# Optimization experiments

Measured on AMD Instinct MI355X. Metric: run time of the kernel, lower is better.

The kernel has to match this reference:

```python
import jax, jax.numpy as jnp
import numpy as np

D, H, L, FF, IN, OUT, S, B = 512, 8, 6, 2048, 32, 3, 512, 32


def setup_inputs() -> dict:
    key = jax.random.key(0)
    ks = iter(jax.random.split(key, 32))
    w = lambda shape: jax.random.normal(next(ks), shape, jnp.float32) * 0.02
    z = lambda shape: jnp.zeros(shape, jnp.float32)
    o = lambda shape: jnp.ones(shape, jnp.float32)
    return {
        'x': jax.random.normal(next(ks), (B, S, IN), jnp.float32),
        'w_in': w((IN, D)), 'b_in': z((D,)), 'g_in': o((D,)), 'be_in': z((D,)),
        'w_qkv': w((L, D, 3 * D)), 'b_qkv': z((L, 3 * D)),
        'w_out': w((L, D, D)), 'b_out': z((L, D)),
        'g1': o((L, D)), 'be1': z((L, D)),
        'w_ff1': w((L, D, FF)), 'b_ff1': z((L, FF)),
        'w_ff2': w((L, FF, D)), 'b_ff2': z((L, D)),
        'g2': o((L, D)), 'be2': z((L, D)),
        'w_h1': w((D, D // 2)), 'b_h1': z((D // 2,)),
        'w_h2': w((D // 2, OUT)), 'b_h2': z((OUT,)),
    }


def _layer_norm(x, g, b, eps=1e-5):
    mu = jnp.mean(x, axis=-1, keepdims=True)
    var = jnp.mean(jnp.square(x - mu), axis=-1, keepdims=True)
    return (x - mu) / jnp.sqrt(var + eps) * g + b


def _gelu(x):
    return jax.nn.gelu(x, approximate=False)  # torch nn.GELU default (erf)


def _pos_encoding(seq_len, d_model):
    pos = jnp.arange(seq_len, dtype=jnp.float32)[:, None]
    div = jnp.exp(jnp.arange(0, d_model, 2, dtype=jnp.float32) * (-np.log(10000.0) / d_model))
    pe = jnp.zeros((seq_len, d_model), jnp.float32)
    pe = pe.at[:, 0::2].set(jnp.sin(pos * div))
    pe = pe.at[:, 1::2].set(jnp.cos(pos * div))
    return pe


def reference(x, w_in, b_in, g_in, be_in, w_qkv, b_qkv, w_out, b_out,
              g1, be1, w_ff1, b_ff1, w_ff2, b_ff2, g2, be2,
              w_h1, b_h1, w_h2, b_h2):
    b, s, _ = x.shape
    d = w_in.shape[1]
    hd = d // H
    scale = hd ** -0.5

    # input projection: Linear -> LayerNorm -> GELU (dropout = identity at eval)
    h = _gelu(_layer_norm(x @ w_in + b_in, g_in, be_in))
    h = h + _pos_encoding(s, d)

    causal_mask = jnp.triu(jnp.ones((s, s), bool), 1)  # True above diagonal = future

    for l in range(w_qkv.shape[0]):
        qkv = (h @ w_qkv[l] + b_qkv[l]).reshape(b, s, 3, H, hd)
        q, k, v = qkv[:, :, 0], qkv[:, :, 1], qkv[:, :, 2]  # [b, s, H, hd]
        scores = jnp.einsum('bihd,bjhd->bhij', q, k) * scale
        scores = jnp.where(causal_mask, -jnp.inf, scores)
        attn = jax.nn.softmax(scores, axis=-1)
        o = jnp.einsum('bhij,bjhd->bihd', attn, v).reshape(b, s, d)
        o = o @ w_out[l] + b_out[l]
        h = _layer_norm(h + o, g1[l], be1[l])
        f = _gelu(h @ w_ff1[l] + b_ff1[l]) @ w_ff2[l] + b_ff2[l]
        h = _layer_norm(h + f, g2[l], be2[l])

    logits = _gelu(h @ w_h1 + b_h1) @ w_h2 + b_h2  # [b, s, OUT]
    return logits[:, -1, :]  # last position only
```

## Files before the change

kernel.cpp:

```cpp
#include <hip/hip_runtime.h>
#include <hip/hip_bf16.h>
#include <math.h>

#define D_   512
#define H_   8
#define HD_  64
#define L_   6
#define FF_  2048
#define IN_  32
#define OUT_ 3
#define S_   512
#define B_   32
#define M_   (B_ * S_)

typedef __attribute__((ext_vector_type(8))) short short8;
typedef __attribute__((ext_vector_type(4))) float floatx4;

__device__ __forceinline__ float gelu_f(float x) {
    const float ax = fabsf(x) * 0.70710678118654752f;
    const float t = __builtin_amdgcn_rcpf(fmaf(0.3275911f, ax, 1.0f));
    float p = fmaf(1.061405429f, t, -1.453152027f);
    p = fmaf(p, t, 1.421413741f);
    p = fmaf(p, t, -0.284496736f);
    p = fmaf(p, t, 0.254829592f);
    p = p * t;
    const float e = __expf(-ax * ax);
    const float er = copysignf(fmaf(-p, e, 1.0f), x);
    return 0.5f * x * (1.0f + er);
}
__device__ __forceinline__ float bf2f(unsigned short u) {
    union { unsigned int i; float f; } c; c.i = ((unsigned)u) << 16; return c.f;
}
__device__ __forceinline__ unsigned short f2bf(float v) {
    __hip_bfloat16 t = __float2bfloat16(v);
    return *(unsigned short*)&t;
}
__device__ __forceinline__ void async16(const void* g, void* l) {
    __builtin_amdgcn_global_load_lds(
        (const __attribute__((address_space(1))) unsigned int*)g,
        (__attribute__((address_space(3))) unsigned int*)l, 16, 0, 0);
}
__device__ __forceinline__ void stage2(const short* g, char* d, long rs, int off2) {
    async16(g, d);
    async16(g + rs, d + off2);
}


#define MFMA_ROW(ai, accr)                                                    \
    accr[0] = __builtin_amdgcn_mfma_f32_16x16x32_bf16(ai, b[0], accr[0], 0, 0, 0); \
    accr[1] = __builtin_amdgcn_mfma_f32_16x16x32_bf16(ai, b[1], accr[1], 0, 0, 0); \
    accr[2] = __builtin_amdgcn_mfma_f32_16x16x32_bf16(ai, b[2], accr[2], 0, 0, 0); \
    accr[3] = __builtin_amdgcn_mfma_f32_16x16x32_bf16(ai, b[3], accr[3], 0, 0, 0);

#define MFMA_PHASE(B0)                                                        \
    __builtin_amdgcn_s_barrier();                                             \
    asm volatile("s_waitcnt lgkmcnt(0)" ::: "memory");                        \
    __builtin_amdgcn_sched_barrier(0);                                        \
    __builtin_amdgcn_s_setprio(1);                                            \
    MFMA_ROW(a[0], acc[B0 + 0])                                               \
    MFMA_ROW(a[1], acc[B0 + 1])                                               \
    MFMA_ROW(a[2], acc[B0 + 2])                                               \
    MFMA_ROW(a[3], acc[B0 + 3])                                               \
    __builtin_amdgcn_s_setprio(0);

template<int DO_GELU, int OUT_BF16, int ADD_RES>
__global__ __launch_bounds__(512, 2)
void gemm_mfma256_k(const __hip_bfloat16* __restrict__ A,
                    const __hip_bfloat16* __restrict__ WT,
                    const float* __restrict__ bias,
                    const float* __restrict__ R,
                    void* __restrict__ C,
                    int N, int K) {
    __shared__ __align__(16) char smem[131072];

    const int tid  = threadIdx.x;
    const int lane = tid & 63;
    const int wave = tid >> 6;

    const int Lid = blockIdx.y * gridDim.x + blockIdx.x;
    const int xcd = Lid & 7;
    const int idx = Lid >> 3;
    const int gx  = gridDim.x, gy8 = gridDim.y >> 3;
    const int m0 = (xcd * gy8 + idx / gx) * 256;
    const int n0 = (idx % gx) * 256;

    const int wm = (wave >> 2) * 128;
    const int wn = (wave & 3) * 64;
    const int r = lane & 15, q = lane >> 4;
    const int qa = (q ^ ((r >> 1) & 3)) * 8;

    const int srow = tid >> 2;
    const int sc = ((tid & 3) ^ ((tid >> 3) & 3)) * 8;
    const short* Ag = (const short*)A + (long)(m0 + srow) * K + sc;
    const short* Bg = (const short*)WT + (long)(n0 + srow) * K + sc;
    const long rs = (long)128 * K;

    floatx4 acc[8][4];
    #pragma unroll
    for (int i = 0; i < 8; i++)
        #pragma unroll
        for (int j = 0; j < 4; j++) acc[i][j] = (floatx4)0.f;

    const int NT = K >> 6;

    stage2(Ag,      smem         + tid * 16, rs, 8192);
    stage2(Bg,      smem + 32768 + tid * 16, rs, 8192);
    stage2(Ag + 32, smem + 16384 + tid * 16, rs, 8192);
    stage2(Bg + 32, smem + 49152 + tid * 16, rs, 8192);
    asm volatile("s_waitcnt vmcnt(4)" ::: "memory");
    __builtin_amdgcn_s_barrier();

    short8 a[4], b[4];
    for (int t = 0; t < NT; ++t) {
        const int cur = t & 1, nxt = cur ^ 1;
        const bool hn = (t + 1 < NT);
        const short* As = (const short*)(smem + cur * 65536);
        const short* Bs = (const short*)(smem + cur * 65536 + 32768);
        const short* Agt = Ag + (t + 1) * 64;
        const short* Bgt = Bg + (t + 1) * 64;
        char* Ad = smem + nxt * 65536;
        char* Bd = smem + nxt * 65536 + 32768;

        #pragma unroll
        for (int i = 0; i < 4; i++)
            a[i] = *(const short8*)&As[(wm + i * 16 + r) * 32 + qa];
        #pragma unroll
        for (int j = 0; j < 4; j++)
            b[j] = *(const short8*)&Bs[(wn + j * 16 + r) * 32 + qa];
        if (hn) stage2(Agt, Ad + tid * 16, rs, 8192);
        MFMA_PHASE(0)
        __builtin_amdgcn_s_barrier();

        #pragma unroll
        for (int i = 0; i < 4; i++)
            a[i] = *(const short8*)&As[(wm + 64 + i * 16 + r) * 32 + qa];
        if (hn) stage2(Bgt, Bd + tid * 16, rs, 8192);
        MFMA_PHASE(4)
        if (hn) asm volatile("s_waitcnt vmcnt(4)" ::: "memory");
        else    asm volatile("s_waitcnt vmcnt(0)" ::: "memory");
        __builtin_amdgcn_s_barrier();

        #pragma unroll
        for (int i = 0; i < 4; i++)
            a[i] = *(const short8*)&As[8192 + (wm + i * 16 + r) * 32 + qa];
        #pragma unroll
        for (int j = 0; j < 4; j++)
            b[j] = *(const short8*)&Bs[8192 + (wn + j * 16 + r) * 32 + qa];
        if (hn) stage2(Agt + 32, Ad + 16384 + tid * 16, rs, 8192);
        MFMA_PHASE(0)
        __builtin_amdgcn_s_barrier();

        #pragma unroll
        for (int i = 0; i < 4; i++)
            a[i] = *(const short8*)&As[8192 + (wm + 64 + i * 16 + r) * 32 + qa];
        if (hn) stage2(Bgt + 32, Bd + 16384 + tid * 16, rs, 8192);
        MFMA_PHASE(4)
        if (hn) asm volatile("s_waitcnt vmcnt(4)" ::: "memory");
        __builtin_amdgcn_s_barrier();
    }

    float* Ef = (float*)smem;
    const int erow = tid >> 3;
    const int ej = tid & 7;
    #pragma unroll
    for (int ch = 0; ch < 4; ch++) {
        __builtin_amdgcn_s_barrier();
        if ((wave >> 2) == (ch >> 1)) {
            #pragma unroll
            for (int mf2 = 0; mf2 < 4; mf2++) {
                const int mf = (ch & 1) * 4 + mf2;
                #pragma unroll
                for (int nf = 0; nf < 4; nf++)
                    #pragma unroll
                    for (int rg = 0; rg < 4; rg++)
                        Ef[(mf2 * 16 + q * 4 + rg) * 260 + wn + nf * 16 + r] =
                            acc[mf][nf][rg];
            }
        }
        __builtin_amdgcn_s_barrier();
        #pragma unroll
        for (int e = 0; e < 8; e++) {
            const int c4 = ej + e * 8;
            const long grow = (long)(m0 + ch * 64 + erow) * N + n0 + c4 * 4;
            const float4 v = *(const float4*)&Ef[erow * 260 + c4 * 4];
            const float4 bv = *(const float4*)&bias[n0 + c4 * 4];
            float o0 = v.x + bv.x, o1 = v.y + bv.y;
            float o2 = v.z + bv.z, o3 = v.w + bv.w;
            if (DO_GELU) {
                o0 = gelu_f(o0); o1 = gelu_f(o1);
                o2 = gelu_f(o2); o3 = gelu_f(o3);
            }
            if (ADD_RES) {
                const float4 rv = *(const float4*)&R[grow];
                o0 += rv.x; o1 += rv.y; o2 += rv.z; o3 += rv.w;
            }
            if (OUT_BF16) {
                ushort4 pk;
                pk.x = f2bf(o0); pk.y = f2bf(o1);
                pk.z = f2bf(o2); pk.w = f2bf(o3);
                *(ushort4*)((unsigned short*)C + grow) = pk;
            } else {
                *(float4*)((float*)C + grow) = make_float4(o0, o1, o2, o3);
            }
        }
    }
}

template<int DO_GELU, int OUT_BF16, int ADD_RES>
__global__ __launch_bounds__(256, 2)
void gemm_mfma_k(const __hip_bfloat16* __restrict__ A,
                 const __hip_bfloat16* __restrict__ WT,
                 const float* __restrict__ bias,
                 const float* __restrict__ R,
                 void* __restrict__ C,
                 int N, int K) {
    __shared__ __align__(16) char smem[65536];
    float* Ep = (float*)smem;

    const int tid  = threadIdx.x;
    const int lane = tid & 63;
    const int wave = tid >> 6;

    const int Lid = blockIdx.y * gridDim.x + blockIdx.x;
    const int xcd = Lid & 7;
    const int idx = Lid >> 3;
    const int gx  = gridDim.x, gy8 = gridDim.y >> 3;
    const int m0 = (xcd * gy8 + idx / gx) * 128;
    const int n0 = (idx % gx) * 128;

    const int wm = (wave >> 1) * 64, wn = (wave & 1) * 64;
    const int r = lane & 15, q = lane >> 4;
    const int qa = (q ^ ((r >> 1) & 3)) * 8;

    const int srow = tid >> 2;
    const int sc = ((tid & 3) ^ ((tid >> 3) & 3)) * 8;
    const short* Ag = (const short*)A + (long)(m0 + srow) * K + sc;
    const short* Bg = (const short*)WT + (long)(n0 + srow) * K + sc;
    const long rs = (long)64 * K;

    floatx4 acc[4][4];
    #pragma unroll
    for (int i = 0; i < 4; i++)
        #pragma unroll
        for (int j = 0; j < 4; j++) acc[i][j] = (floatx4)0.f;

    const int NT = K >> 6;

    stage2(Ag,      smem + 0     + tid * 16, rs, 4096);
    stage2(Bg,      smem + 16384 + tid * 16, rs, 4096);
    stage2(Ag + 32, smem + 8192  + tid * 16, rs, 4096);
    stage2(Bg + 32, smem + 24576 + tid * 16, rs, 4096);
    asm volatile("s_waitcnt vmcnt(4)" ::: "memory");
    __builtin_amdgcn_s_barrier();
    __builtin_amdgcn_sched_barrier(0);

    short8 a[4], b[4];
    for (int t = 0; t < NT; ++t) {
        const int cur = t & 1, nxt = cur ^ 1;
        const bool hn = (t + 1 < NT);
        const short* As = (const short*)(smem + cur * 32768);
        const short* Bs = (const short*)(smem + cur * 32768 + 16384);
        const short* Agt = Ag + (t + 1) * 64;
        const short* Bgt = Bg + (t + 1) * 64;
        char* Ad = smem + nxt * 32768;
        char* Bd = smem + nxt * 32768 + 16384;

        if (hn) {
            stage2(Agt, Ad + tid * 16, rs, 4096);
            stage2(Bgt, Bd + tid * 16, rs, 4096);
        }
        #pragma unroll
        for (int i = 0; i < 4; i++)
            a[i] = *(const short8*)&As[(wm + i * 16 + r) * 32 + qa];
        #pragma unroll
        for (int j = 0; j < 4; j++)
            b[j] = *(const short8*)&Bs[(wn + j * 16 + r) * 32 + qa];
        #pragma unroll
        for (int i = 0; i < 4; i++)
            #pragma unroll
            for (int j = 0; j < 4; j++)
                acc[i][j] = __builtin_amdgcn_mfma_f32_16x16x32_bf16(
                    a[i], b[j], acc[i][j], 0, 0, 0);
        __builtin_amdgcn_sched_barrier(0);
        if (hn) asm volatile("s_waitcnt vmcnt(4)" ::: "memory");
        else    asm volatile("s_waitcnt vmcnt(0)" ::: "memory");
        __builtin_amdgcn_s_barrier();
        __builtin_amdgcn_sched_barrier(0);

        if (hn) {
            stage2(Agt + 32, Ad + 8192 + tid * 16, rs, 4096);
            stage2(Bgt + 32, Bd + 8192 + tid * 16, rs, 4096);
        }
        #pragma unroll
        for (int i = 0; i < 4; i++)
            a[i] = *(const short8*)&As[4096 + (wm + i * 16 + r) * 32 + qa];
        #pragma unroll
        for (int j = 0; j < 4; j++)
            b[j] = *(const short8*)&Bs[4096 + (wn + j * 16 + r) * 32 + qa];
        #pragma unroll
        for (int i = 0; i < 4; i++)
            #pragma unroll
            for (int j = 0; j < 4; j++)
                acc[i][j] = __builtin_amdgcn_mfma_f32_16x16x32_bf16(
                    a[i], b[j], acc[i][j], 0, 0, 0);
        __builtin_amdgcn_sched_barrier(0);
        if (hn) asm volatile("s_waitcnt vmcnt(4)" ::: "memory");
        __builtin_amdgcn_s_barrier();
        __builtin_amdgcn_sched_barrier(0);
    }

    const int erow = tid >> 5;
    const int ecol = (tid & 31) * 4;
    const float4 bvec = *(const float4*)&bias[n0 + ecol];

    #pragma unroll
    for (int pass = 0; pass < 2; pass++) {
        if (pass) __syncthreads();
        if ((wave >> 1) == pass) {
            #pragma unroll
            for (int i = 0; i < 4; i++)
                #pragma unroll
                for (int j = 0; j < 4; j++)
                    #pragma unroll
                    for (int rg = 0; rg < 4; rg++)
                        Ep[(i * 16 + q * 4 + rg) * 132 + wn + j * 16 + r] =
                            acc[i][j][rg];
        }
        __syncthreads();
        #pragma unroll
        for (int it = 0; it < 8; it++) {
            const int row = it * 8 + erow;
            const long grow = (long)(m0 + pass * 64 + row) * N + n0 + ecol;
            const float4 v = *(const float4*)&Ep[row * 132 + ecol];
            float o0 = v.x + bvec.x, o1 = v.y + bvec.y;
            float o2 = v.z + bvec.z, o3 = v.w + bvec.w;
            if (DO_GELU) {
                o0 = gelu_f(o0); o1 = gelu_f(o1);
                o2 = gelu_f(o2); o3 = gelu_f(o3);
            }
            if (ADD_RES) {
                const float4 rv = *(const float4*)&R[grow];
                o0 += rv.x; o1 += rv.y; o2 += rv.z; o3 += rv.w;
            }
            if (OUT_BF16) {
                ushort4 pk;
                pk.x = f2bf(o0); pk.y = f2bf(o1);
                pk.z = f2bf(o2); pk.w = f2bf(o3);
                *(ushort4*)((unsigned short*)C + grow) = pk;
            } else {
                *(float4*)((float*)C + grow) = make_float4(o0, o1, o2, o3);
            }
        }
    }
}

__global__ __launch_bounds__(512, 1)
void gemm_ln_k(const __hip_bfloat16* __restrict__ A,
               const __hip_bfloat16* __restrict__ WT,
               const float* __restrict__ bias,
               const float* R,
               const float* __restrict__ g,
               const float* __restrict__ be,
               float* Hout,
               __hip_bfloat16* __restrict__ Hb,
               int K) {
    __shared__ __align__(16) char smem[147456];
    const int tid  = threadIdx.x;
    const int lane = tid & 63;
    const int wave = tid >> 6;

    const int Lid = blockIdx.x;
    const int m0 = ((Lid & 7) * 32 + (Lid >> 3)) * 64;

    const int wm2 = wave >> 2;
    const int wn4 = wave & 3;
    const int r = lane & 15, q = lane >> 4;
    const int qaB  = (q ^ ((r >> 1) & 3)) * 8;
    const int qaA0 = ((q)     ^ (r & 7)) * 8;
    const int qaA1 = ((4 + q) ^ (r & 7)) * 8;

    const int arow = tid >> 3;
    const int asb  = ((tid & 7) ^ ((tid >> 3) & 7)) * 8;
    const short* Ag = (const short*)A + (long)(m0 + arow) * K + asb;
    const int brow = tid >> 2;
    const int bsb  = ((tid & 3) ^ ((tid >> 3) & 3)) * 8;
    const short* Bg = (const short*)WT + (long)brow * K + bsb;
    const long brs = (long)128 * K;

    floatx4 acc[2][8];
    #pragma unroll
    for (int i = 0; i < 2; i++)
        #pragma unroll
        for (int j = 0; j < 8; j++) acc[i][j] = (floatx4)0.f;

    const int NTT = K >> 6;

    {
        char* base = smem;
        async16(Ag, base + tid * 16);
        const short* p0 = Bg;
        char* d0 = base + 8192 + tid * 16;
        async16(p0, d0); async16(p0 + brs, d0 + 8192);
        async16(p0 + 2 * brs, d0 + 16384); async16(p0 + 3 * brs, d0 + 24576);
        const short* p1 = Bg + 32;
        char* d1 = base + 40960 + tid * 16;
        async16(p1, d1); async16(p1 + brs, d1 + 8192);
        async16(p1 + 2 * brs, d1 + 16384); async16(p1 + 3 * brs, d1 + 24576);
    }
    asm volatile("s_waitcnt vmcnt(4)" ::: "memory");
    __builtin_amdgcn_s_barrier();
    __builtin_amdgcn_sched_barrier(0);

    for (int t = 0; t < NTT; ++t) {
        const int cur = t & 1, nxt = cur ^ 1;
        const bool hn = (t + 1 < NTT);
        const short* As  = (const short*)(smem + cur * 73728);
        const short* B0s = (const short*)(smem + cur * 73728 + 8192);
        const short* B1s = (const short*)(smem + cur * 73728 + 40960);
        char* nb = smem + nxt * 73728;
        const long k1 = (long)(t + 1) * 64;

        if (hn) {
            async16(Ag + k1, nb + tid * 16);
            const short* p0 = Bg + k1;
            char* d0 = nb + 8192 + tid * 16;
            async16(p0, d0); async16(p0 + brs, d0 + 8192);
            async16(p0 + 2 * brs, d0 + 16384); async16(p0 + 3 * brs, d0 + 24576);
        }
        {
            short8 a0 = *(const short8*)&As[(wm2 * 32 +      r) * 64 + qaA0];
            short8 a1 = *(const short8*)&As[(wm2 * 32 + 16 + r) * 64 + qaA0];
            short8 b[8];
            #pragma unroll
            for (int nf = 0; nf < 8; nf++)
                b[nf] = *(const short8*)&B0s[(wn4 * 128 + nf * 16 + r) * 32 + qaB];
            #pragma unroll
            for (int nf = 0; nf < 8; nf++) {
                acc[0][nf] = __builtin_amdgcn_mfma_f32_16x16x32_bf16(a0, b[nf], acc[0][nf], 0, 0, 0);
                acc[1][nf] = __builtin_amdgcn_mfma_f32_16x16x32_bf16(a1, b[nf], acc[1][nf], 0, 0, 0);
            }
        }
        __builtin_amdgcn_sched_barrier(0);
        if (hn) asm volatile("s_waitcnt vmcnt(4)" ::: "memory");
        else    asm volatile("s_waitcnt vmcnt(0)" ::: "memory");
        __builtin_amdgcn_s_barrier();
        __builtin_amdgcn_sched_barrier(0);

        if (hn) {
            const short* p1 = Bg + k1 + 32;
            char* d1 = nb + 40960 + tid * 16;
            async16(p1, d1); async16(p1 + brs, d1 + 8192);
            async16(p1 + 2 * brs, d1 + 16384); async16(p1 + 3 * brs, d1 + 24576);
        }
        {
            short8 a0 = *(const short8*)&As[(wm2 * 32 +      r) * 64 + qaA1];
            short8 a1 = *(const short8*)&As[(wm2 * 32 + 16 + r) * 64 + qaA1];
            short8 b[8];
            #pragma unroll
            for (int nf = 0; nf < 8; nf++)
                b[nf] = *(const short8*)&B1s[(wn4 * 128 + nf * 16 + r) * 32 + qaB];
            #pragma unroll
            for (int nf = 0; nf < 8; nf++) {
                acc[0][nf] = __builtin_amdgcn_mfma_f32_16x16x32_bf16(a0, b[nf], acc[0][nf], 0, 0, 0);
                acc[1][nf] = __builtin_amdgcn_mfma_f32_16x16x32_bf16(a1, b[nf], acc[1][nf], 0, 0, 0);
            }
        }
        __builtin_amdgcn_sched_barrier(0);
        if (hn) asm volatile("s_waitcnt vmcnt(4)" ::: "memory");
        __builtin_amdgcn_s_barrier();
        __builtin_amdgcn_sched_barrier(0);
    }

    float* Ef = (float*)smem;
    float* stat = (float*)(smem + 66816);
    const float gl = g[tid], bl = be[tid], bv = bias[tid];

    #pragma unroll
    for (int ch = 0; ch < 2; ch++) {
        if (ch) __syncthreads();
        if (wm2 == ch) {
            #pragma unroll
            for (int mf = 0; mf < 2; mf++)
                #pragma unroll
                for (int nf = 0; nf < 8; nf++)
                    #pragma unroll
                    for (int rg = 0; rg < 4; rg++)
                        Ef[(mf * 16 + q * 4 + rg) * 522 + wn4 * 128 + nf * 16 + r] =
                            acc[mf][nf][rg];
        }
        __syncthreads();
        const int gm = m0 + ch * 32;
        #pragma unroll 8
        for (int k = 0; k < 32; k++)
            Ef[k * 522 + tid] += bv + R[(long)(gm + k) * 512 + tid];
        __syncthreads();
        {
            const int row = tid >> 4, cc = tid & 15;
            float s = 0.f, ss = 0.f;
            #pragma unroll 8
            for (int j = 0; j < 32; j++) {
                const float v = Ef[row * 522 + cc + 16 * j];
                s += v; ss += v * v;
            }
            #pragma unroll
            for (int off = 1; off < 16; off <<= 1) {
                s  += __shfl_xor(s, off);
                ss += __shfl_xor(ss, off);
            }
            const float mu  = s * (1.0f / 512.0f);
            const float var = fmaxf(ss * (1.0f / 512.0f) - mu * mu, 0.f);
            const float inv = 1.0f / sqrtf(var + 1e-5f);
            if (cc == 0) { stat[row * 2] = mu; stat[row * 2 + 1] = inv; }
        }
        __syncthreads();
        #pragma unroll 8
        for (int k = 0; k < 32; k++) {
            const float v  = Ef[k * 522 + tid];
            const float o  = (v - stat[k * 2]) * stat[k * 2 + 1] * gl + bl;
            const long idx = (long)(gm + k) * 512 + tid;
            Hout[idx] = o;
            ((unsigned short*)Hb)[idx] = f2bf(o);
        }
    }
}

__global__ __launch_bounds__(256)
void transpose_cast_k(const float* __restrict__ W, __hip_bfloat16* __restrict__ WT,
                      int K, int N) {
    __shared__ float tile[32][33];
    const float* Wl = W + (long)blockIdx.z * K * N;
    __hip_bfloat16* WTl = WT + (long)blockIdx.z * K * N;
    const int n0 = blockIdx.x * 32, k0 = blockIdx.y * 32;
    const int tx = threadIdx.x & 31, ty = threadIdx.x >> 5;
    for (int rr = ty; rr < 32; rr += 8)
        tile[rr][tx] = Wl[(long)(k0 + rr) * N + n0 + tx];
    __syncthreads();
    for (int rr = ty; rr < 32; rr += 8)
        WTl[(long)(n0 + rr) * K + k0 + tx] = __float2bfloat16(tile[tx][rr]);
}

template<int DO_GELU>
__global__ __launch_bounds__(256)
void gemm_bias_k(const float* __restrict__ A, long lda,
                 const float* __restrict__ W,
                 const float* __restrict__ bias,
                 float* __restrict__ C,
                 int M, int N, int K) {
    __shared__ float As[16][64];
    __shared__ float Ws[16][64];
    const int tx = threadIdx.x;
    const int ty = threadIdx.y;
    const int tid = ty * 16 + tx;
    const int m0 = blockIdx.y * 64;
    const int n0 = blockIdx.x * 64;
    float acc[4][4] = {};
    for (int k0 = 0; k0 < K; k0 += 16) {
        #pragma unroll
        for (int e = tid; e < 64 * 16; e += 256) {
            int m = e >> 4, k = e & 15;
            float v = 0.f;
            if (m0 + m < M) v = A[(long)(m0 + m) * lda + k0 + k];
            As[k][m] = v;
        }
        #pragma unroll
        for (int e = tid; e < 16 * 64; e += 256) {
            int k = e >> 6, n = e & 63;
            float v = 0.f;
            if (n0 + n < N) v = W[(long)(k0 + k) * N + n0 + n];
            Ws[k][n] = v;
        }
        __syncthreads();
        #pragma unroll
        for (int kk = 0; kk < 16; kk++) {
            float a[4], w[4];
            #pragma unroll
            for (int i = 0; i < 4; i++) a[i] = As[kk][ty * 4 + i];
            #pragma unroll
            for (int j = 0; j < 4; j++) w[j] = Ws[kk][tx * 4 + j];
            #pragma unroll
            for (int i = 0; i < 4; i++)
                #pragma unroll
                for (int j = 0; j < 4; j++)
                    acc[i][j] += a[i] * w[j];
        }
        __syncthreads();
    }
    #pragma unroll
    for (int i = 0; i < 4; i++) {
        int m = m0 + ty * 4 + i;
        if (m >= M) continue;
        #pragma unroll
        for (int j = 0; j < 4; j++) {
            int n = n0 + tx * 4 + j;
            if (n >= N) continue;
            float v = acc[i][j] + bias[n];
            if (DO_GELU) v = gelu_f(v);
            C[(long)m * N + n] = v;
        }
    }
}

__global__ __launch_bounds__(256)
void ln_k(const float* __restrict__ X,
          const float* __restrict__ g,
          const float* __restrict__ be,
          float* __restrict__ H,
          __hip_bfloat16* __restrict__ Hb) {
    const int row = blockIdx.x * 4 + (threadIdx.x >> 6);
    const int lane = threadIdx.x & 63;
    const float* xp = X + (long)row * D_ + lane * 8;
    const float4 a = *(const float4*)xp;
    const float4 c = *(const float4*)(xp + 4);
    float s = a.x + a.y + a.z + a.w + c.x + c.y + c.z + c.w;
    #pragma unroll
    for (int off = 1; off < 64; off <<= 1) s += __shfl_xor(s, off);
    const float mu = s * (1.0f / D_);
    float d[8] = { a.x - mu, a.y - mu, a.z - mu, a.w - mu,
                   c.x - mu, c.y - mu, c.z - mu, c.w - mu };
    float ss = 0.f;
    #pragma unroll
    for (int e = 0; e < 8; e++) ss += d[e] * d[e];
    #pragma unroll
    for (int off = 1; off < 64; off <<= 1) ss += __shfl_xor(ss, off);
    const float inv = 1.0f / sqrtf(ss * (1.0f / D_) + 1e-5f);
    const float4 g0 = *(const float4*)(g + lane * 8);
    const float4 g1 = *(const float4*)(g + lane * 8 + 4);
    const float4 e0 = *(const float4*)(be + lane * 8);
    const float4 e1 = *(const float4*)(be + lane * 8 + 4);
    const float gv[8] = { g0.x, g0.y, g0.z, g0.w, g1.x, g1.y, g1.z, g1.w };
    const float ev[8] = { e0.x, e0.y, e0.z, e0.w, e1.x, e1.y, e1.z, e1.w };
    float o[8];
    short8 pk;
    #pragma unroll
    for (int e = 0; e < 8; e++) {
        o[e] = d[e] * inv * gv[e] + ev[e];
        pk[e] = (short)f2bf(o[e]);
    }
    float* hp = H + (long)row * D_ + lane * 8;
    *(float4*)hp = make_float4(o[0], o[1], o[2], o[3]);
    *(float4*)(hp + 4) = make_float4(o[4], o[5], o[6], o[7]);
    *(short8*)((unsigned short*)Hb + (long)row * D_ + lane * 8) = pk;
}

__global__ __launch_bounds__(256)
void ln_gelu_pos_k(const float* __restrict__ X,
                   const float* __restrict__ g,
                   const float* __restrict__ be,
                   float* __restrict__ Hout,
                   __hip_bfloat16* __restrict__ Hb) {
    const int row = blockIdx.x;
    const int s = row & (S_ - 1);
    const int t = threadIdx.x;
    const float* x = X + (long)row * D_;
    float v0 = x[t], v1 = x[t + 256];
    __shared__ float red[256];
    red[t] = v0 + v1;
    __syncthreads();
    for (int off = 128; off; off >>= 1) {
        if (t < off) red[t] += red[t + off];
        __syncthreads();
    }
    float mu = red[0] * (1.0f / D_);
    __syncthreads();
    float d0 = v0 - mu, d1 = v1 - mu;
    red[t] = d0 * d0 + d1 * d1;
    __syncthreads();
    for (int off = 128; off; off >>= 1) {
        if (t < off) red[t] += red[t + off];
        __syncthreads();
    }
    float var = red[0] * (1.0f / D_);
    float inv = 1.0f / sqrtf(var + 1e-5f);
    float o0 = gelu_f(d0 * inv * g[t] + be[t]);
    float o1 = gelu_f(d1 * inv * g[t + 256] + be[t + 256]);
    {
        int d = t, i = d >> 1;
        float dv = expf((float)(2 * i) * (-9.210340371976184f / 512.0f));
        float ang = (float)s * dv;
        o0 += (d & 1) ? cosf(ang) : sinf(ang);
    }
    {
        int d = t + 256, i = d >> 1;
        float dv = expf((float)(2 * i) * (-9.210340371976184f / 512.0f));
        float ang = (float)s * dv;
        o1 += (d & 1) ? cosf(ang) : sinf(ang);
    }
    Hout[(long)row * D_ + t] = o0;
    Hout[(long)row * D_ + t + 256] = o1;
    Hb[(long)row * D_ + t] = __float2bfloat16(o0);
    Hb[(long)row * D_ + t + 256] = __float2bfloat16(o1);
}

#define LDT 72
__global__ __launch_bounds__(256)
void attn_mfma_k(const __hip_bfloat16* __restrict__ qkv,
                 __hip_bfloat16* __restrict__ O) {
    const int qt = blockIdx.x;
    const int bh = blockIdx.y;
    const int b = bh >> 3, h = bh & (H_ - 1);
    const int tid = threadIdx.x;
    const int wave = tid >> 6, lane = tid & 63;
    const int ln = lane & 15, quad = lane >> 4;
    const int wm = wave * 32;
    const int i0 = qt * 128;

    __shared__ unsigned short Qs[128 * LDT];
    __shared__ unsigned short Ks[64 * LDT];
    __shared__ unsigned short Vt[64 * LDT];
    __shared__ unsigned short Ps[128 * LDT];
    __shared__ float stat[128];

    const unsigned short* base = (const unsigned short*)qkv + (long)b * S_ * (3 * D_);

    {
        const int r0 = tid >> 3, c0 = (tid & 7) * 8;
        #pragma unroll
        for (int i = 0; i < 4; i++) {
            const int rw = i * 32 + r0;
            *(short8*)&Qs[rw * LDT + c0] =
                *(const short8*)(base + (long)(i0 + rw) * (3 * D_) + h * HD_ + c0);
        }
    }

    float m_i[2] = { -INFINITY, -INFINITY };
    float l_i[2] = { 0.f, 0.f };
    floatx4 o_acc[2][4];
    #pragma unroll
    for (int i = 0; i < 2; i++)
        #pragma unroll
        for (int j = 0; j < 4; j++) o_acc[i][j] = (floatx4)0.f;

    const int kr = tid >> 2, kc = (tid & 3) * 16;
    const int vj = tid & 63, vc = (tid >> 6) * 16;

    const int ktmax = 2 * qt + 1;
    for (int kt = 0; kt <= ktmax; kt++) {
        const int j0 = kt * 64;
        {
            const unsigned short* kp = base + (long)(j0 + kr) * (3 * D_) + D_ + h * HD_ + kc;
            *(short8*)&Ks[kr * LDT + kc]     = *(const short8*)(kp);
            *(short8*)&Ks[kr * LDT + kc + 8] = *(const short8*)(kp + 8);
            const unsigned short* vp = base + (long)(j0 + vj) * (3 * D_) + 2 * D_ + h * HD_ + vc;
            short8 v0 = *(const short8*)(vp);
            short8 v1 = *(const short8*)(vp + 8);
            #pragma unroll
            for (int e = 0; e < 8; e++) {
                Vt[(vc + e) * LDT + vj]     = (unsigned short)v0[e];
                Vt[(vc + 8 + e) * LDT + vj] = (unsigned short)v1[e];
            }
        }
        __syncthreads();

        floatx4 sa[4][2];
        #pragma unroll
        for (int mt = 0; mt < 4; mt++)
            #pragma unroll
            for (int nt = 0; nt < 2; nt++) sa[mt][nt] = (floatx4)0.f;
        #pragma unroll
        for (int c = 0; c < 2; c++) {
            short8 kf[4], qf[2];
            #pragma unroll
            for (int mt = 0; mt < 4; mt++)
                kf[mt] = *(const short8*)&Ks[(mt * 16 + ln) * LDT + c * 32 + quad * 8];
            #pragma unroll
            for (int nt = 0; nt < 2; nt++)
                qf[nt] = *(const short8*)&Qs[(wm + nt * 16 + ln) * LDT + c * 32 + quad * 8];
            #pragma unroll
            for (int mt = 0; mt < 4; mt++)
                #pragma unroll
                for (int nt = 0; nt < 2; nt++)
                    sa[mt][nt] = __builtin_amdgcn_mfma_f32_16x16x32_bf16(
                        kf[mt], qf[nt], sa[mt][nt], 0, 0, 0);
        }

        const bool domask = (kt >= 2 * qt);
        #pragma unroll
        for (int nt = 0; nt < 2; nt++) {
            const int qg = i0 + wm + nt * 16 + ln;
            float mx = -INFINITY;
            #pragma unroll
            for (int mt = 0; mt < 4; mt++)
                #pragma unroll
                for (int rg = 0; rg < 4; rg++) {
                    float v = sa[mt][nt][rg] * 0.125f;
                    if (domask && (j0 + mt * 16 + quad * 4 + rg > qg)) v = -INFINITY;
                    sa[mt][nt][rg] = v;
                    mx = fmaxf(mx, v);
                }
            mx = fmaxf(mx, __shfl_xor(mx, 16));
            mx = fmaxf(mx, __shfl_xor(mx, 32));
            const float mn = fmaxf(m_i[nt], mx);
            const float alpha = __expf(m_i[nt] - mn);
            m_i[nt] = mn;
            float ls = 0.f;
            #pragma unroll
            for (int mt = 0; mt < 4; mt++) {
                ushort4 pk;
                float p0 = __expf(sa[mt][nt][0] - mn);
                float p1 = __expf(sa[mt][nt][1] - mn);
                float p2 = __expf(sa[mt][nt][2] - mn);
                float p3 = __expf(sa[mt][nt][3] - mn);
                ls += p0 + p1 + p2 + p3;
                pk.x = f2bf(p0); pk.y = f2bf(p1); pk.z = f2bf(p2); pk.w = f2bf(p3);
                *(ushort4*)&Ps[(wm + nt * 16 + ln) * LDT + mt * 16 + quad * 4] = pk;
            }
            ls += __shfl_xor(ls, 16);
            ls += __shfl_xor(ls, 32);
            l_i[nt] = l_i[nt] * alpha + ls;
            if (quad == 0) stat[wm + nt * 16 + ln] = alpha;
        }

        #pragma unroll
        for (int mt2 = 0; mt2 < 2; mt2++) {
            #pragma unroll
            for (int rg = 0; rg < 4; rg++) {
                const float a = stat[wm + mt2 * 16 + quad * 4 + rg];
                #pragma unroll
                for (int nt = 0; nt < 4; nt++) o_acc[mt2][nt][rg] *= a;
            }
        }

        #pragma unroll
        for (int c = 0; c < 2; c++) {
            short8 pf[2], vf[4];
            #pragma unroll
            for (int mt2 = 0; mt2 < 2; mt2++)
                pf[mt2] = *(const short8*)&Ps[(wm + mt2 * 16 + ln) * LDT + c * 32 + quad * 8];
            #pragma unroll
            for (int nt = 0; nt < 4; nt++)
                vf[nt] = *(const short8*)&Vt[(nt * 16 + ln) * LDT + c * 32 + quad * 8];
            #pragma unroll
            for (int mt2 = 0; mt2 < 2; mt2++)
                #pragma unroll
                for (int nt = 0; nt < 4; nt++)
                    o_acc[mt2][nt] = __builtin_amdgcn_mfma_f32_16x16x32_bf16(
                        pf[mt2], vf[nt], o_acc[mt2][nt], 0, 0, 0);
        }
        __syncthreads();
    }

    if (quad == 0) {
        stat[wm + ln]      = l_i[0];
        stat[wm + 16 + ln] = l_i[1];
    }
    unsigned short* Og = (unsigned short*)O;
    #pragma unroll
    for (int mt2 = 0; mt2 < 2; mt2++) {
        #pragma unroll
        for (int rg = 0; rg < 4; rg++) {
            const float linv = 1.0f / stat[wm + mt2 * 16 + quad * 4 + rg];
            const long row = (long)(b * S_ + i0 + wm + mt2 * 16 + quad * 4 + rg);
            #pragma unroll
            for (int nt = 0; nt < 4; nt++)
                Og[row * D_ + h * HD_ + nt * 16 + ln] =
                    f2bf(o_acc[mt2][nt][rg] * linv);
        }
    }
}

__global__ __launch_bounds__(256)
void head1_k(const float* __restrict__ h, const float* __restrict__ w1,
             const float* __restrict__ b1, float* __restrict__ th) {
    __shared__ float hs[D_];
    const int b = blockIdx.x, n = threadIdx.x;
    const float* hr = h + (long)(b * S_ + S_ - 1) * D_;
    hs[n] = hr[n];
    hs[n + 256] = hr[n + 256];
    __syncthreads();
    float s = 0.f;
    #pragma unroll 8
    for (int k = 0; k < D_; k++) s += hs[k] * w1[(long)k * 256 + n];
    th[b * 256 + n] = gelu_f(s + b1[n]);
}

__global__ __launch_bounds__(64)
void head2_k(const float* __restrict__ th, const float* __restrict__ w2,
             const float* __restrict__ b2, float* __restrict__ out) {
    const int b = blockIdx.x, lane = threadIdx.x;
    const float* t = th + b * 256;
    float s0 = 0.f, s1 = 0.f, s2 = 0.f;
    #pragma unroll
    for (int e = 0; e < 4; e++) {
        const int k = lane * 4 + e;
        const float tv = t[k];
        s0 += tv * w2[k * 3 + 0];
        s1 += tv * w2[k * 3 + 1];
        s2 += tv * w2[k * 3 + 2];
    }
    #pragma unroll
    for (int off = 1; off < 64; off <<= 1) {
        s0 += __shfl_xor(s0, off);
        s1 += __shfl_xor(s1, off);
        s2 += __shfl_xor(s2, off);
    }
    if (lane == 0) {
        out[b * 3 + 0] = s0 + b2[0];
        out[b * 3 + 1] = s1 + b2[1];
        out[b * 3 + 2] = s2 + b2[2];
    }
}

extern "C" void kernel_launch(void* const* d_in, const int* in_sizes, int n_in,
                              void* d_out, int out_size, void* d_ws, size_t ws_size,
                              hipStream_t stream) {
    const float* x     = (const float*)d_in[0];
    const float* w_in  = (const float*)d_in[1];
    const float* b_in  = (const float*)d_in[2];
    const float* g_in  = (const float*)d_in[3];
    const float* be_in = (const float*)d_in[4];
    const float* w_qkv = (const float*)d_in[5];
    const float* b_qkv = (const float*)d_in[6];
    const float* w_out = (const float*)d_in[7];
    const float* b_out = (const float*)d_in[8];
    const float* g1    = (const float*)d_in[9];
    const float* be1   = (const float*)d_in[10];
    const float* w_ff1 = (const float*)d_in[11];
    const float* b_ff1 = (const float*)d_in[12];
    const float* w_ff2 = (const float*)d_in[13];
    const float* b_ff2 = (const float*)d_in[14];
    const float* g2    = (const float*)d_in[15];
    const float* be2   = (const float*)d_in[16];
    const float* w_h1  = (const float*)d_in[17];
    const float* b_h1  = (const float*)d_in[18];
    const float* w_h2  = (const float*)d_in[19];
    const float* b_h2  = (const float*)d_in[20];
    float* out = (float*)d_out;

    float* h    = (float*)d_ws;
    float* bufB = h + (long)M_ * D_;
    float* th   = bufB + (long)M_ * D_;
    __hip_bfloat16* hb    = (__hip_bfloat16*)(th + 32 * 256);
    __hip_bfloat16* attb  = hb + (long)M_ * D_;
    __hip_bfloat16* bufAb = attb + (long)M_ * D_;
    __hip_bfloat16* qkvT  = bufAb + (long)M_ * FF_;
    __hip_bfloat16* outT  = qkvT + (long)L_ * (3 * D_) * D_;
    __hip_bfloat16* ff1T  = outT + (long)L_ * D_ * D_;
    __hip_bfloat16* ff2T  = ff1T + (long)L_ * FF_ * D_;

    dim3 blk(16, 16);

    transpose_cast_k<<<dim3((3 * D_) / 32, D_ / 32, L_), 256, 0, stream>>>(w_qkv, qkvT, D_, 3 * D_);
    transpose_cast_k<<<dim3(D_ / 32, D_ / 32, L_), 256, 0, stream>>>(w_out, outT, D_, D_);
    transpose_cast_k<<<dim3(FF_ / 32, D_ / 32, L_), 256, 0, stream>>>(w_ff1, ff1T, D_, FF_);
    transpose_cast_k<<<dim3(D_ / 32, FF_ / 32, L_), 256, 0, stream>>>(w_ff2, ff2T, FF_, D_);

    gemm_bias_k<0><<<dim3(D_ / 64, M_ / 64), blk, 0, stream>>>(
        x, IN_, w_in, b_in, bufB, M_, D_, IN_);
    ln_gelu_pos_k<<<M_, 256, 0, stream>>>(bufB, g_in, be_in, h, hb);

    for (int l = 0; l < L_; l++) {
        gemm_mfma_k<0, 1, 0><<<dim3((3 * D_) / 128, M_ / 128), 256, 0, stream>>>(
            hb, qkvT + (long)l * (3 * D_) * D_, b_qkv + l * 3 * D_, nullptr,
            bufAb, 3 * D_, D_);
        attn_mfma_k<<<dim3(S_ / 128, B_ * H_), 256, 0, stream>>>(bufAb, attb);
        gemm_ln_k<<<256, 512, 0, stream>>>(
            attb, outT + (long)l * D_ * D_, b_out + l * D_, h,
            g1 + l * D_, be1 + l * D_, h, hb, D_);
        gemm_mfma256_k<1, 1, 0><<<dim3(FF_ / 256, M_ / 256), 512, 0, stream>>>(
            hb, ff1T + (long)l * FF_ * D_, b_ff1 + l * FF_, nullptr,
            bufAb, FF_, D_);
        gemm_ln_k<<<256, 512, 0, stream>>>(
            bufAb, ff2T + (long)l * D_ * FF_, b_ff2 + l * D_, h,
            g2 + l * D_, be2 + l * D_, h, hb, FF_);
    }

    head1_k<<<B_, 256, 0, stream>>>(h, w_h1, b_h1, th);
    head2_k<<<B_, 64, 0, stream>>>(th, w_h2, b_h2, out);
}
```

Before: 1.638 ms.

## Retile fused GEMM+LayerNorm to 4x4 per-wave fragments and revert FF1 to 128-tile GEMM

The fused GEMM+LayerNorm kernel now gives each of its 8 waves a 64-column strip across all 64 rows, using a 4x4 grid of MFMA fragments instead of 2x8. This lets the epilogue stage the whole 64x512 tile in shared memory in one pass, with a single LayerNorm sweep where there were two 32-row chunks. The FF1 projection drops the 256x256 tiled GEMM and goes back to the 128x128 gemm_mfma_k, and the unused ln_k kernel is deleted. The aim is better fragment reuse and fewer barriers in the epilogue, at the cost of more shared memory per block (about 132 KB) and a smaller tile for FF1.

```diff
diff --git a/kernel.cpp b/kernel.cpp
--- a/kernel.cpp
+++ b/kernel.cpp
@@ -45,166 +45,6 @@
     async16(g + rs, d + off2);
 }
 
-
-#define MFMA_ROW(ai, accr)                                                    \
-    accr[0] = __builtin_amdgcn_mfma_f32_16x16x32_bf16(ai, b[0], accr[0], 0, 0, 0); \
-    accr[1] = __builtin_amdgcn_mfma_f32_16x16x32_bf16(ai, b[1], accr[1], 0, 0, 0); \
-    accr[2] = __builtin_amdgcn_mfma_f32_16x16x32_bf16(ai, b[2], accr[2], 0, 0, 0); \
-    accr[3] = __builtin_amdgcn_mfma_f32_16x16x32_bf16(ai, b[3], accr[3], 0, 0, 0);
-
-#define MFMA_PHASE(B0)                                                        \
-    __builtin_amdgcn_s_barrier();                                             \
-    asm volatile("s_waitcnt lgkmcnt(0)" ::: "memory");                        \
-    __builtin_amdgcn_sched_barrier(0);                                        \
-    __builtin_amdgcn_s_setprio(1);                                            \
-    MFMA_ROW(a[0], acc[B0 + 0])                                               \
-    MFMA_ROW(a[1], acc[B0 + 1])                                               \
-    MFMA_ROW(a[2], acc[B0 + 2])                                               \
-    MFMA_ROW(a[3], acc[B0 + 3])                                               \
-    __builtin_amdgcn_s_setprio(0);
-
-template<int DO_GELU, int OUT_BF16, int ADD_RES>
-__global__ __launch_bounds__(512, 2)
-void gemm_mfma256_k(const __hip_bfloat16* __restrict__ A,
-                    const __hip_bfloat16* __restrict__ WT,
-                    const float* __restrict__ bias,
-                    const float* __restrict__ R,
-                    void* __restrict__ C,
-                    int N, int K) {
-    __shared__ __align__(16) char smem[131072];
-
-    const int tid  = threadIdx.x;
-    const int lane = tid & 63;
-    const int wave = tid >> 6;
-
-    const int Lid = blockIdx.y * gridDim.x + blockIdx.x;
-    const int xcd = Lid & 7;
-    const int idx = Lid >> 3;
-    const int gx  = gridDim.x, gy8 = gridDim.y >> 3;
-    const int m0 = (xcd * gy8 + idx / gx) * 256;
-    const int n0 = (idx % gx) * 256;
-
-    const int wm = (wave >> 2) * 128;
-    const int wn = (wave & 3) * 64;
-    const int r = lane & 15, q = lane >> 4;
-    const int qa = (q ^ ((r >> 1) & 3)) * 8;
-
-    const int srow = tid >> 2;
-    const int sc = ((tid & 3) ^ ((tid >> 3) & 3)) * 8;
-    const short* Ag = (const short*)A + (long)(m0 + srow) * K + sc;
-    const short* Bg = (const short*)WT + (long)(n0 + srow) * K + sc;
-    const long rs = (long)128 * K;
-
-    floatx4 acc[8][4];
-    #pragma unroll
-    for (int i = 0; i < 8; i++)
-        #pragma unroll
-        for (int j = 0; j < 4; j++) acc[i][j] = (floatx4)0.f;
-
-    const int NT = K >> 6;
-
-    stage2(Ag,      smem         + tid * 16, rs, 8192);
-    stage2(Bg,      smem + 32768 + tid * 16, rs, 8192);
-    stage2(Ag + 32, smem + 16384 + tid * 16, rs, 8192);
-    stage2(Bg + 32, smem + 49152 + tid * 16, rs, 8192);
-    asm volatile("s_waitcnt vmcnt(4)" ::: "memory");
-    __builtin_amdgcn_s_barrier();
-
-    short8 a[4], b[4];
-    for (int t = 0; t < NT; ++t) {
-        const int cur = t & 1, nxt = cur ^ 1;
-        const bool hn = (t + 1 < NT);
-        const short* As = (const short*)(smem + cur * 65536);
-        const short* Bs = (const short*)(smem + cur * 65536 + 32768);
-        const short* Agt = Ag + (t + 1) * 64;
-        const short* Bgt = Bg + (t + 1) * 64;
-        char* Ad = smem + nxt * 65536;
-        char* Bd = smem + nxt * 65536 + 32768;
-
-        #pragma unroll
-        for (int i = 0; i < 4; i++)
-            a[i] = *(const short8*)&As[(wm + i * 16 + r) * 32 + qa];
-        #pragma unroll
-        for (int j = 0; j < 4; j++)
-            b[j] = *(const short8*)&Bs[(wn + j * 16 + r) * 32 + qa];
-        if (hn) stage2(Agt, Ad + tid * 16, rs, 8192);
-        MFMA_PHASE(0)
-        __builtin_amdgcn_s_barrier();
-
-        #pragma unroll
-        for (int i = 0; i < 4; i++)
-            a[i] = *(const short8*)&As[(wm + 64 + i * 16 + r) * 32 + qa];
-        if (hn) stage2(Bgt, Bd + tid * 16, rs, 8192);
-        MFMA_PHASE(4)
-        if (hn) asm volatile("s_waitcnt vmcnt(4)" ::: "memory");
-        else    asm volatile("s_waitcnt vmcnt(0)" ::: "memory");
-        __builtin_amdgcn_s_barrier();
-
-        #pragma unroll
-        for (int i = 0; i < 4; i++)
-            a[i] = *(const short8*)&As[8192 + (wm + i * 16 + r) * 32 + qa];
-        #pragma unroll
-        for (int j = 0; j < 4; j++)
-            b[j] = *(const short8*)&Bs[8192 + (wn + j * 16 + r) * 32 + qa];
-        if (hn) stage2(Agt + 32, Ad + 16384 + tid * 16, rs, 8192);
-        MFMA_PHASE(0)
-        __builtin_amdgcn_s_barrier();
-
-        #pragma unroll
-        for (int i = 0; i < 4; i++)
-            a[i] = *(const short8*)&As[8192 + (wm + 64 + i * 16 + r) * 32 + qa];
-        if (hn) stage2(Bgt + 32, Bd + 16384 + tid * 16, rs, 8192);
-        MFMA_PHASE(4)
-        if (hn) asm volatile("s_waitcnt vmcnt(4)" ::: "memory");
-        __builtin_amdgcn_s_barrier();
-    }
-
-    float* Ef = (float*)smem;
-    const int erow = tid >> 3;
-    const int ej = tid & 7;
-    #pragma unroll
-    for (int ch = 0; ch < 4; ch++) {
-        __builtin_amdgcn_s_barrier();
-        if ((wave >> 2) == (ch >> 1)) {
-            #pragma unroll
-            for (int mf2 = 0; mf2 < 4; mf2++) {
-                const int mf = (ch & 1) * 4 + mf2;
-                #pragma unroll
-                for (int nf = 0; nf < 4; nf++)
-                    #pragma unroll
-                    for (int rg = 0; rg < 4; rg++)
-                        Ef[(mf2 * 16 + q * 4 + rg) * 260 + wn + nf * 16 + r] =
-                            acc[mf][nf][rg];
-            }
-        }
-        __builtin_amdgcn_s_barrier();
-        #pragma unroll
-        for (int e = 0; e < 8; e++) {
-            const int c4 = ej + e * 8;
-            const long grow = (long)(m0 + ch * 64 + erow) * N + n0 + c4 * 4;
-            const float4 v = *(const float4*)&Ef[erow * 260 + c4 * 4];
-            const float4 bv = *(const float4*)&bias[n0 + c4 * 4];
-            float o0 = v.x + bv.x, o1 = v.y + bv.y;
-            float o2 = v.z + bv.z, o3 = v.w + bv.w;
-            if (DO_GELU) {
-                o0 = gelu_f(o0); o1 = gelu_f(o1);
-                o2 = gelu_f(o2); o3 = gelu_f(o3);
-            }
-            if (ADD_RES) {
-                const float4 rv = *(const float4*)&R[grow];
-                o0 += rv.x; o1 += rv.y; o2 += rv.z; o3 += rv.w;
-            }
-            if (OUT_BF16) {
-                ushort4 pk;
-                pk.x = f2bf(o0); pk.y = f2bf(o1);
-                pk.z = f2bf(o2); pk.w = f2bf(o3);
-                *(ushort4*)((unsigned short*)C + grow) = pk;
-            } else {
-                *(float4*)((float*)C + grow) = make_float4(o0, o1, o2, o3);
-            }
-        }
-    }
-}
 
 template<int DO_GELU, int OUT_BF16, int ADD_RES>
 __global__ __launch_bounds__(256, 2)
@@ -372,12 +212,11 @@
     const int Lid = blockIdx.x;
     const int m0 = ((Lid & 7) * 32 + (Lid >> 3)) * 64;
 
-    const int wm2 = wave >> 2;
-    const int wn4 = wave & 3;
     const int r = lane & 15, q = lane >> 4;
     const int qaB  = (q ^ ((r >> 1) & 3)) * 8;
     const int qaA0 = ((q)     ^ (r & 7)) * 8;
     const int qaA1 = ((4 + q) ^ (r & 7)) * 8;
+    const int wn = wave * 64;
 
     const int arow = tid >> 3;
     const int asb  = ((tid & 7) ^ ((tid >> 3) & 7)) * 8;
@@ -387,11 +226,11 @@
     const short* Bg = (const short*)WT + (long)brow * K + bsb;
     const long brs = (long)128 * K;
 
-    floatx4 acc[2][8];
-    #pragma unroll
-    for (int i = 0; i < 2; i++)
-        #pragma unroll
-        for (int j = 0; j < 8; j++) acc[i][j] = (floatx4)0.f;
+    floatx4 acc[4][4];
+    #pragma unroll
+    for (int i = 0; i < 4; i++)
+        #pragma unroll
+        for (int j = 0; j < 4; j++) acc[i][j] = (floatx4)0.f;
 
     const int NTT = K >> 6;
 
@@ -428,17 +267,19 @@
             async16(p0 + 2 * brs, d0 + 16384); async16(p0 + 3 * brs, d0 + 24576);
         }
         {
-            short8 a0 = *(const short8*)&As[(wm2 * 32 +      r) * 64 + qaA0];
-            short8 a1 = *(const short8*)&As[(wm2 * 32 + 16 + r) * 64 + qaA0];
-            short8 b[8];
-            #pragma unroll
-            for (int nf = 0; nf < 8; nf++)
-                b[nf] = *(const short8*)&B0s[(wn4 * 128 + nf * 16 + r) * 32 + qaB];
-            #pragma unroll
-            for (int nf = 0; nf < 8; nf++) {
-                acc[0][nf] = __builtin_amdgcn_mfma_f32_16x16x32_bf16(a0, b[nf], acc[0][nf], 0, 0, 0);
-                acc[1][nf] = __builtin_amdgcn_mfma_f32_16x16x32_bf16(a1, b[nf], acc[1][nf], 0, 0, 0);
-            }
+            short8 a[4], b[4];
+            #pragma unroll
+            for (int mf = 0; mf < 4; mf++)
+                a[mf] = *(const short8*)&As[(mf * 16 + r) * 64 + qaA0];
+            #pragma unroll
+            for (int nf = 0; nf < 4; nf++)
+                b[nf] = *(const short8*)&B0s[(wn + nf * 16 + r) * 32 + qaB];
+            #pragma unroll
+            for (int mf = 0; mf < 4; mf++)
+                #pragma unroll
+                for (int nf = 0; nf < 4; nf++)
+                    acc[mf][nf] = __builtin_amdgcn_mfma_f32_16x16x32_bf16(
+                        a[mf], b[nf], acc[mf][nf], 0, 0, 0);
         }
         __builtin_amdgcn_sched_barrier(0);
         if (hn) asm volatile("s_waitcnt vmcnt(4)" ::: "memory");
@@ -453,17 +294,19 @@
             async16(p1 + 2 * brs, d1 + 16384); async16(p1 + 3 * brs, d1 + 24576);
         }
         {
-            short8 a0 = *(const short8*)&As[(wm2 * 32 +      r) * 64 + qaA1];
-            short8 a1 = *(const short8*)&As[(wm2 * 32 + 16 + r) * 64 + qaA1];
-            short8 b[8];
-            #pragma unroll
-            for (int nf = 0; nf < 8; nf++)
-                b[nf] = *(const short8*)&B1s[(wn4 * 128 + nf * 16 + r) * 32 + qaB];
-            #pragma unroll
-            for (int nf = 0; nf < 8; nf++) {
-                acc[0][nf] = __builtin_amdgcn_mfma_f32_16x16x32_bf16(a0, b[nf], acc[0][nf], 0, 0, 0);
-                acc[1][nf] = __builtin_amdgcn_mfma_f32_16x16x32_bf16(a1, b[nf], acc[1][nf], 0, 0, 0);
-            }
+            short8 a[4], b[4];
+            #pragma unroll
+            for (int mf = 0; mf < 4; mf++)
+                a[mf] = *(const short8*)&As[(mf * 16 + r) * 64 + qaA1];
+            #pragma unroll
+            for (int nf = 0; nf < 4; nf++)
+                b[nf] = *(const short8*)&B1s[(wn + nf * 16 + r) * 32 + qaB];
+            #pragma unroll
+            for (int mf = 0; mf < 4; mf++)
+                #pragma unroll
+                for (int nf = 0; nf < 4; nf++)
+                    acc[mf][nf] = __builtin_amdgcn_mfma_f32_16x16x32_bf16(
+                        a[mf], b[nf], acc[mf][nf], 0, 0, 0);
         }
         __builtin_amdgcn_sched_barrier(0);
         if (hn) asm volatile("s_waitcnt vmcnt(4)" ::: "memory");
@@ -472,55 +315,48 @@
     }
 
     float* Ef = (float*)smem;
-    float* stat = (float*)(smem + 66816);
+    float* stat = (float*)(smem + 132096);
     const float gl = g[tid], bl = be[tid], bv = bias[tid];
 
     #pragma unroll
-    for (int ch = 0; ch < 2; ch++) {
-        if (ch) __syncthreads();
-        if (wm2 == ch) {
-            #pragma unroll
-            for (int mf = 0; mf < 2; mf++)
-                #pragma unroll
-                for (int nf = 0; nf < 8; nf++)
-                    #pragma unroll
-                    for (int rg = 0; rg < 4; rg++)
-                        Ef[(mf * 16 + q * 4 + rg) * 522 + wn4 * 128 + nf * 16 + r] =
-                            acc[mf][nf][rg];
-        }
-        __syncthreads();
-        const int gm = m0 + ch * 32;
+    for (int mf = 0; mf < 4; mf++)
+        #pragma unroll
+        for (int nf = 0; nf < 4; nf++)
+            #pragma unroll
+            for (int rg = 0; rg < 4; rg++)
+                Ef[(mf * 16 + q * 4 + rg) * 516 + wn + nf * 16 + r] =
+                    acc[mf][nf][rg];
+    __syncthreads();
+    #pragma unroll 8
+    for (int k = 0; k < 64; k++)
+        Ef[k * 516 + tid] += bv + R[(long)(m0 + k) * 512 + tid];
+    __syncthreads();
+    {
+        const int row = tid >> 3, cc = tid & 7;
+        float s = 0.f, ss = 0.f;
         #pragma unroll 8
-        for (int k = 0; k < 32; k++)
-            Ef[k * 522 + tid] += bv + R[(long)(gm + k) * 512 + tid];
-        __syncthreads();
-        {
-            const int row = tid >> 4, cc = tid & 15;
-            float s = 0.f, ss = 0.f;
-            #pragma unroll 8
-            for (int j = 0; j < 32; j++) {
-                const float v = Ef[row * 522 + cc + 16 * j];
-                s += v; ss += v * v;
-            }
-            #pragma unroll
-            for (int off = 1; off < 16; off <<= 1) {
-                s  += __shfl_xor(s, off);
-                ss += __shfl_xor(ss, off);
-            }
-            const float mu  = s * (1.0f / 512.0f);
-            const float var = fmaxf(ss * (1.0f / 512.0f) - mu * mu, 0.f);
-            const float inv = 1.0f / sqrtf(var + 1e-5f);
-            if (cc == 0) { stat[row * 2] = mu; stat[row * 2 + 1] = inv; }
-        }
-        __syncthreads();
-        #pragma unroll 8
-        for (int k = 0; k < 32; k++) {
-            const float v  = Ef[k * 522 + tid];
-            const float o  = (v - stat[k * 2]) * stat[k * 2 + 1] * gl + bl;
-            const long idx = (long)(gm + k) * 512 + tid;
-            Hout[idx] = o;
-            ((unsigned short*)Hb)[idx] = f2bf(o);
-        }
+        for (int j = 0; j < 64; j++) {
+            const float v = Ef[row * 516 + cc + 8 * j];
+            s += v; ss += v * v;
+        }
+        #pragma unroll
+        for (int off = 1; off < 8; off <<= 1) {
+            s  += __shfl_xor(s, off);
+            ss += __shfl_xor(ss, off);
+        }
+        const float mu  = s * (1.0f / 512.0f);
+        const float var = fmaxf(ss * (1.0f / 512.0f) - mu * mu, 0.f);
+        const float inv = 1.0f / sqrtf(var + 1e-5f);
+        if (cc == 0) { stat[row * 2] = mu; stat[row * 2 + 1] = inv; }
+    }
+    __syncthreads();
+    #pragma unroll 8
+    for (int k = 0; k < 64; k++) {
+        const float v  = Ef[k * 516 + tid];
+        const float o  = (v - stat[k * 2]) * stat[k * 2 + 1] * gl + bl;
+        const long idx = (long)(m0 + k) * 512 + tid;
+        Hout[idx] = o;
+        ((unsigned short*)Hb)[idx] = f2bf(o);
     }
 }
 
@@ -598,48 +434,6 @@
             C[(long)m * N + n] = v;
         }
     }
-}
-
-__global__ __launch_bounds__(256)
-void ln_k(const float* __restrict__ X,
-          const float* __restrict__ g,
-          const float* __restrict__ be,
-          float* __restrict__ H,
-          __hip_bfloat16* __restrict__ Hb) {
-    const int row = blockIdx.x * 4 + (threadIdx.x >> 6);
-    const int lane = threadIdx.x & 63;
-    const float* xp = X + (long)row * D_ + lane * 8;
-    const float4 a = *(const float4*)xp;
-    const float4 c = *(const float4*)(xp + 4);
-    float s = a.x + a.y + a.z + a.w + c.x + c.y + c.z + c.w;
-    #pragma unroll
-    for (int off = 1; off < 64; off <<= 1) s += __shfl_xor(s, off);
-    const float mu = s * (1.0f / D_);
-    float d[8] = { a.x - mu, a.y - mu, a.z - mu, a.w - mu,
-                   c.x - mu, c.y - mu, c.z - mu, c.w - mu };
-    float ss = 0.f;
-    #pragma unroll
-    for (int e = 0; e < 8; e++) ss += d[e] * d[e];
-    #pragma unroll
-    for (int off = 1; off < 64; off <<= 1) ss += __shfl_xor(ss, off);
-    const float inv = 1.0f / sqrtf(ss * (1.0f / D_) + 1e-5f);
-    const float4 g0 = *(const float4*)(g + lane * 8);
-    const float4 g1 = *(const float4*)(g + lane * 8 + 4);
-    const float4 e0 = *(const float4*)(be + lane * 8);
-    const float4 e1 = *(const float4*)(be + lane * 8 + 4);
-    const float gv[8] = { g0.x, g0.y, g0.z, g0.w, g1.x, g1.y, g1.z, g1.w };
-    const float ev[8] = { e0.x, e0.y, e0.z, e0.w, e1.x, e1.y, e1.z, e1.w };
-    float o[8];
-    short8 pk;
-    #pragma unroll
-    for (int e = 0; e < 8; e++) {
-        o[e] = d[e] * inv * gv[e] + ev[e];
-        pk[e] = (short)f2bf(o[e]);
-    }
-    float* hp = H + (long)row * D_ + lane * 8;
-    *(float4*)hp = make_float4(o[0], o[1], o[2], o[3]);
-    *(float4*)(hp + 4) = make_float4(o[4], o[5], o[6], o[7]);
-    *(short8*)((unsigned short*)Hb + (long)row * D_ + lane * 8) = pk;
 }
 
 __global__ __launch_bounds__(256)
@@ -956,7 +750,7 @@
         gemm_ln_k<<<256, 512, 0, stream>>>(
             attb, outT + (long)l * D_ * D_, b_out + l * D_, h,
             g1 + l * D_, be1 + l * D_, h, hb, D_);
-        gemm_mfma256_k<1, 1, 0><<<dim3(FF_ / 256, M_ / 256), 512, 0, stream>>>(
+        gemm_mfma_k<1, 1, 0><<<dim3(FF_ / 128, M_ / 128), 256, 0, stream>>>(
             hb, ff1T + (long)l * FF_ * D_, b_ff1 + l * FF_, nullptr,
             bufAb, FF_, D_);
         gemm_ln_k<<<256, 512, 0, stream>>>(
```

Result: faster. 1.592 ms (-2.8%).
